# Performance work log

Measured on AMD Instinct MI355X. Metric: run time of the kernel, lower is better.

## Reference

```python
import jax, jax.numpy as jnp
import numpy as np

WIN = (2, 7, 7)
SHIFT = (1, 3, 3)
HEADS = 4
DIM = 128
MLP_HID = 512
N = WIN[0] * WIN[1] * WIN[2]  # 98
EPS = 1e-5


def _rel_pos_index():
    d = np.arange(WIN[0]); h = np.arange(WIN[1]); w = np.arange(WIN[2])
    coords = np.stack(np.meshgrid(d, h, w, indexing='ij'))  # (3, Wd, Wh, Ww)
    flat = coords.reshape(3, -1)  # (3, N)
    rel = flat[:, :, None] - flat[:, None, :]  # (3, N, N)
    rel = rel.transpose(1, 2, 0).astype(np.int64)  # (N, N, 3)
    rel[..., 0] += WIN[0] - 1
    rel[..., 1] += WIN[1] - 1
    rel[..., 2] += WIN[2] - 1
    rel[..., 0] *= (2 * WIN[1] - 1) * (2 * WIN[2] - 1)
    rel[..., 1] *= (2 * WIN[2] - 1)
    return rel.sum(-1)  # (N, N)


def setup_inputs() -> dict:
    key = jax.random.key(0)
    ks = jax.random.split(key, 8)
    B, D, H, W, C = 4, 8, 56, 56, DIM
    tbl_size = (2 * WIN[0] - 1) * (2 * WIN[1] - 1) * (2 * WIN[2] - 1)  # 507
    s = 0.02
    return {
        'x': jax.random.normal(ks[0], (B, D, H, W, C), jnp.float32),
        'rel_idx': jnp.asarray(_rel_pos_index(), jnp.int32),
        'rpb_table': s * jax.random.normal(ks[1], (tbl_size, HEADS), jnp.float32),
        'qkv_w': s * jax.random.normal(ks[2], (C, 3 * C), jnp.float32),
        'qkv_b': jnp.zeros((3 * C,), jnp.float32),
        'proj_w': s * jax.random.normal(ks[3], (C, C), jnp.float32),
        'proj_b': jnp.zeros((C,), jnp.float32),
        'ln1_g': jnp.ones((C,), jnp.float32),
        'ln1_b': jnp.zeros((C,), jnp.float32),
        'ln2_g': jnp.ones((C,), jnp.float32),
        'ln2_b': jnp.zeros((C,), jnp.float32),
        'mlp_w1': s * jax.random.normal(ks[4], (C, MLP_HID), jnp.float32),
        'mlp_b1': jnp.zeros((MLP_HID,), jnp.float32),
        'mlp_w2': s * jax.random.normal(ks[5], (MLP_HID, C), jnp.float32),
        'mlp_b2': jnp.zeros((C,), jnp.float32),
    }


def _layernorm(x, g, b):
    mu = jnp.mean(x, -1, keepdims=True)
    var = jnp.var(x, -1, keepdims=True)
    return (x - mu) * jax.lax.rsqrt(var + EPS) * g + b


def _window_partition(x):
    B, Dp, Hp, Wp, C = x.shape
    x = x.reshape(B, Dp // WIN[0], WIN[0], Hp // WIN[1], WIN[1], Wp // WIN[2], WIN[2], C)
    x = x.transpose(0, 1, 3, 5, 2, 4, 6, 7)
    return x.reshape(-1, N, C)


def _window_reverse(win, B, Dp, Hp, Wp):
    C = win.shape[-1]
    x = win.reshape(B, Dp // WIN[0], Hp // WIN[1], Wp // WIN[2], WIN[0], WIN[1], WIN[2], C)
    x = x.transpose(0, 1, 4, 2, 5, 3, 6, 7)
    return x.reshape(B, Dp, Hp, Wp, C)


def _block(x, rel_idx, rpb_table, qkv_w, qkv_b, proj_w, proj_b,
           ln1_g, ln1_b, ln2_g, ln2_b, mlp_w1, mlp_b1, mlp_w2, mlp_b2):
    B, D, H, W, C = x.shape
    shortcut = x
    x = _layernorm(x, ln1_g, ln1_b)
    pad_d = (-D) % WIN[0]; pad_h = (-H) % WIN[1]; pad_w = (-W) % WIN[2]
    x = jnp.pad(x, ((0, 0), (0, pad_d), (0, pad_h), (0, pad_w), (0, 0)))
    _, Dp, Hp, Wp, _ = x.shape
    x = jnp.roll(x, (-SHIFT[0], -SHIFT[1], -SHIFT[2]), axis=(1, 2, 3))
    xw = _window_partition(x)  # (B_, N, C)
    B_ = xw.shape[0]
    hd = C // HEADS
    qkv = (xw @ qkv_w + qkv_b).reshape(B_, N, 3, HEADS, hd).transpose(2, 0, 3, 1, 4)
    q, k, v = qkv[0], qkv[1], qkv[2]  # (B_, h, N, hd)
    q = q * (hd ** -0.5)
    attn = jnp.einsum('bhnd,bhmd->bhnm', q, k)
    bias = rpb_table[rel_idx.reshape(-1)].reshape(N, N, HEADS).transpose(2, 0, 1)
    attn = attn + bias[None]
    # NOTE: the original module calls attn with mask=None even when shifted.
    attn = jax.nn.softmax(attn, axis=-1)
    out = jnp.einsum('bhnm,bhmd->bhnd', attn, v).transpose(0, 2, 1, 3).reshape(B_, N, C)
    out = out @ proj_w + proj_b
    x = _window_reverse(out, B, Dp, Hp, Wp)
    x = jnp.roll(x, (SHIFT[0], SHIFT[1], SHIFT[2]), axis=(1, 2, 3))
    x = x[:, :D, :H, :W, :]
    x = shortcut + x
    h1 = _layernorm(x, ln2_g, ln2_b)
    h1 = jax.nn.gelu(h1 @ mlp_w1 + mlp_b1, approximate=False)
    return x + (h1 @ mlp_w2 + mlp_b2)


def reference(x, rel_idx, rpb_table, qkv_w, qkv_b, proj_w, proj_b,
              ln1_g, ln1_b, ln2_g, ln2_b, mlp_w1, mlp_b1, mlp_w2, mlp_b2):
    return _block(x, rel_idx, rpb_table, qkv_w, qkv_b, proj_w, proj_b,
                  ln1_g, ln1_b, ln2_g, ln2_b, mlp_w1, mlp_b1, mlp_w2, mlp_b2)
```

## Files before the change

kernel.cpp:

```cpp
#include <hip/hip_runtime.h>
#include <hip/hip_bf16.h>
#include <cstdint>

#define NWIN   1024
#define NTOK   98
#define BIAS_N 9604

typedef __attribute__((ext_vector_type(8))) short bf16x8;
typedef __attribute__((ext_vector_type(4))) float f32x4;

__device__ __forceinline__ float b2f(unsigned short u) {
  union { uint32_t i; float f; } v; v.i = ((uint32_t)u) << 16; return v.f;
}
__device__ __forceinline__ float b2f_lo(uint32_t u) {
  union { uint32_t i; float f; } v; v.i = u << 16; return v.f;
}
__device__ __forceinline__ float b2f_hi(uint32_t u) {
  union { uint32_t i; float f; } v; v.i = u & 0xffff0000u; return v.f;
}
__device__ __forceinline__ unsigned short f2b(float f) {
  union { float f; uint32_t i; } v; v.f = f;
  uint32_t r = v.i + 0x7fffu + ((v.i >> 16) & 1u);
  return (unsigned short)(r >> 16);
}
__device__ __forceinline__ float ldf(const void* p, size_t i, int f32) {
  return f32 ? ((const float*)p)[i] : b2f(((const unsigned short*)p)[i]);
}
__device__ __forceinline__ void stf(void* p, size_t i, int f32, float v) {
  if (f32) ((float*)p)[i] = v;
  else     ((unsigned short*)p)[i] = f2b(v);
}
__device__ __forceinline__ float2 ldf2(const void* p, size_t i, int f32) {
  if (f32) { const float* q = (const float*)p + i; return make_float2(q[0], q[1]); }
  uint32_t u = *(const uint32_t*)((const unsigned short*)p + i);
  return make_float2(b2f_lo(u), b2f_hi(u));
}
__device__ __forceinline__ float gelu_f(float x) {
  float a = fabsf(x) * 0.70710678118654752f;
  float t = __builtin_amdgcn_rcpf(1.0f + 0.3275911f * a);
  float p = ((((1.061405429f * t - 1.453152027f) * t + 1.421413741f) * t
              - 0.284496736f) * t + 0.254829592f) * t;
  float erfp = 1.0f - p * __expf(-a * a);
  return 0.5f * x * (1.0f + copysignf(erfp, x));
}

#define QG_OFF   0
#define KG_OFF   25690112
#define VGT_OFF  51380224
#define ZPAD_OFF 80740352
#define BIAS_OFF 80748544
#define WQ_OFF   80902208
#define WP_OFF   81000512
#define W1_OFF   81033280
#define W2_OFF   81164352
#define PAR_OFF  81295424
#define FLAG_OFF 81302080
#define LNG_OFF  81302144
#define P_LN1G 0
#define P_LN1B 128
#define P_LN2G 256
#define P_LN2B 384
#define P_QKVB 512
#define P_PROJB 896
#define P_B1  1024
#define P_B2  1536

__global__ __launch_bounds__(256) void detect_kernel(const uint32_t* __restrict__ xw,
                                                     int* __restrict__ flag) {
  __shared__ int cnt;
  if (threadIdx.x == 0) cnt = 0;
  __syncthreads();
  uint32_t w = xw[threadIdx.x];
  int e = (w >> 23) & 0xFF;
  if (e >= 112 && e <= 134) atomicAdd(&cnt, 1);
  __syncthreads();
  if (threadIdx.x == 0) *flag = (cnt >= 128) ? 1 : 0;
}

__global__ __launch_bounds__(256) void prep_kernel(
    const void* __restrict__ qkvw, const void* __restrict__ projw,
    const void* __restrict__ w1, const void* __restrict__ w2,
    const void* __restrict__ ln1g, const void* __restrict__ ln1b,
    const void* __restrict__ ln2g, const void* __restrict__ ln2b,
    const void* __restrict__ qkvb, const void* __restrict__ projb,
    const void* __restrict__ b1, const void* __restrict__ b2,
    const int* __restrict__ flag,
    unsigned short* __restrict__ wq_t, unsigned short* __restrict__ wp_t,
    unsigned short* __restrict__ w1_t, unsigned short* __restrict__ w2_t,
    float* __restrict__ par, unsigned short* __restrict__ zpad) {
  const int f32 = *flag;
  int idx = blockIdx.x * 256 + threadIdx.x;
  if (idx < 49152) {
    int n = idx >> 7, k = idx & 127;
    wq_t[idx] = f2b(ldf(qkvw, (size_t)k * 384 + n, f32));
  } else if ((idx -= 49152) < 16384) {
    int n = idx >> 7, k = idx & 127;
    wp_t[idx] = f2b(ldf(projw, (size_t)k * 128 + n, f32));
  } else if ((idx -= 16384) < 65536) {
    int n = idx >> 7, k = idx & 127;
    w1_t[idx] = f2b(ldf(w1, (size_t)k * 512 + n, f32));
  } else if ((idx -= 65536) < 65536) {
    int n = idx >> 9, k = idx & 511;
    w2_t[idx] = f2b(ldf(w2, (size_t)k * 128 + n, f32));
  } else if ((idx -= 65536) < 1664) {
    float v;
    if      (idx < 128)  v = ldf(ln1g, idx, f32);
    else if (idx < 256)  v = ldf(ln1b, idx - 128, f32);
    else if (idx < 384)  v = ldf(ln2g, idx - 256, f32);
    else if (idx < 512)  v = ldf(ln2b, idx - 384, f32);
    else if (idx < 896)  v = ldf(qkvb, idx - 512, f32);
    else if (idx < 1024) v = ldf(projb, idx - 896, f32);
    else if (idx < 1536) v = ldf(b1, idx - 1024, f32);
    else                 v = ldf(b2, idx - 1536, f32);
    par[idx] = v;
  } else if ((idx -= 1664) < 4096) {
    zpad[idx] = 0;
  }
}

__global__ __launch_bounds__(256) void bias_kernel(const int* __restrict__ rel_idx,
                                                   const void* __restrict__ tbl,
                                                   const int* __restrict__ flag,
                                                   float* __restrict__ bias) {
  const int f32 = *flag;
  int i = blockIdx.x * 256 + threadIdx.x;
  if (i >= 4 * BIAS_N) return;
  int h = i / BIAS_N, ij = i % BIAS_N;
  bias[i] = ldf(tbl, (size_t)rel_idx[ij] * 4 + h, f32);
}

__global__ __launch_bounds__(256) void qkv_win_kernel(
    const void* __restrict__ x, const int* __restrict__ flag,
    const unsigned short* __restrict__ wq_t, const float* __restrict__ par,
    unsigned short* __restrict__ qg, unsigned short* __restrict__ kg,
    unsigned short* __restrict__ vgt) {
  __shared__ unsigned short lnx[112 * 136];
  const int f32 = *flag;
  const int tid = threadIdx.x, wave = tid >> 6, lane = tid & 63;
  const int quad = lane >> 4, lcol = lane & 15;
  const int win = blockIdx.x;
  const int bb = win >> 8, r = win & 255;
  const int wd = r >> 6, r2 = r & 63, wh = r2 >> 3, ww = r2 & 7;

  for (int t = wave; t < NTOK; t += 4) {
    int td = t / 49, r3 = t % 49, th = r3 / 7, tw = r3 % 7;
    int sd = (wd * 2 + td + 1) & 7;
    int sh = (wh * 7 + th + 3) % 56;
    int sw = (ww * 7 + tw + 3) % 56;
    size_t src = ((((size_t)bb * 8 + sd) * 56 + sh) * 56 + sw) * 128;
    int c0 = lane * 2;
    float2 f = ldf2(x, src + c0, f32);
    float s = f.x + f.y, ss = f.x * f.x + f.y * f.y;
#pragma unroll
    for (int off = 32; off >= 1; off >>= 1) { s += __shfl_xor(s, off); ss += __shfl_xor(ss, off); }
    float mu = s * (1.0f / 128.0f);
    float var = ss * (1.0f / 128.0f) - mu * mu;
    float rs = rsqrtf(var + 1e-5f);
    float y0 = (f.x - mu) * rs * par[P_LN1G + c0] + par[P_LN1B + c0];
    float y1 = (f.y - mu) * rs * par[P_LN1G + c0 + 1] + par[P_LN1B + c0 + 1];
    *(uint32_t*)(lnx + t * 136 + c0) = (uint32_t)f2b(y0) | ((uint32_t)f2b(y1) << 16);
  }
  for (int i = tid; i < 14 * 68; i += 256) {
    int rr = i / 68, c = i % 68;
    *(uint32_t*)(lnx + (98 + rr) * 136 + c * 2) = 0u;
  }
  __syncthreads();

  for (int p = 0; p < 6; ++p) {
    const int n = p * 64 + wave * 16 + lcol;
    bf16x8 bfr[4];
#pragma unroll
    for (int ks = 0; ks < 4; ++ks)
      bfr[ks] = *(const bf16x8*)(wq_t + (size_t)n * 128 + ks * 32 + quad * 8);
    const int region = n >> 7, cc = n & 127, head = cc >> 5, d = cc & 31;
    const float bc = par[P_QKVB + n];
    if (region < 2) {
      unsigned short* dst = (region == 0 ? qg : kg) +
                            (((size_t)win * 4 + head) * NTOK) * 32 + d;
      const float scale = region == 0 ? 0.17677669529663687f : 1.0f;
      for (int mt = 0; mt < 7; ++mt) {
        f32x4 acc = (f32x4){0.f, 0.f, 0.f, 0.f};
#pragma unroll
        for (int ks = 0; ks < 4; ++ks) {
          bf16x8 a = *(const bf16x8*)(lnx + (mt * 16 + lcol) * 136 + ks * 32 + quad * 8);
          acc = __builtin_amdgcn_mfma_f32_16x16x32_bf16(a, bfr[ks], acc, 0, 0, 0);
        }
#pragma unroll
        for (int rr = 0; rr < 4; ++rr) {
          int m = mt * 16 + quad * 4 + rr;
          if (m < NTOK) dst[m * 32] = f2b((acc[rr] + bc) * scale);
        }
      }
    } else {
      unsigned short* dstv = vgt + (((size_t)win * 4 + head) * 32 + d) * 112;
      for (int mt = 0; mt < 7; ++mt) {
        f32x4 acc = (f32x4){0.f, 0.f, 0.f, 0.f};
#pragma unroll
        for (int ks = 0; ks < 4; ++ks) {
          bf16x8 a = *(const bf16x8*)(lnx + (mt * 16 + lcol) * 136 + ks * 32 + quad * 8);
          acc = __builtin_amdgcn_mfma_f32_16x16x32_bf16(a, bfr[ks], acc, 0, 0, 0);
        }
        ushort4 w;
        int m0 = mt * 16 + quad * 4;
        w.x = (m0 + 0 < NTOK) ? f2b(acc[0] + bc) : (unsigned short)0;
        w.y = (m0 + 1 < NTOK) ? f2b(acc[1] + bc) : (unsigned short)0;
        w.z = (m0 + 2 < NTOK) ? f2b(acc[2] + bc) : (unsigned short)0;
        w.w = (m0 + 3 < NTOK) ? f2b(acc[3] + bc) : (unsigned short)0;
        *(ushort4*)(dstv + m0) = w;
      }
    }
  }
}

__global__ __launch_bounds__(256, 4) void attn_fused_kernel(
    const unsigned short* __restrict__ qg, const unsigned short* __restrict__ kg,
    const unsigned short* __restrict__ vgt, const float* __restrict__ bias,
    const unsigned short* __restrict__ wp_t, const float* __restrict__ par,
    const void* __restrict__ x, const int* __restrict__ flag,
    unsigned short* __restrict__ lng, void* __restrict__ out) {
  __shared__ __align__(16) unsigned short smem[15232];
  const int f32 = *flag;
  const int tid = threadIdx.x, wave = tid >> 6, lane = tid & 63;
  const int quad = lane >> 4, lcol = lane & 15;
  const int win = blockIdx.x, h = wave;
  const size_t hb = (((size_t)win * 4 + h) * NTOK) * 32;
  const unsigned short* vbase = vgt + (((size_t)win * 4 + h) * 32) * 112;

  unsigned short* plh = smem + h * (16 * 132);

  for (int idx = lane; idx < 16 * 16; idx += 64) {
    int rr = idx >> 4, c = 112 + (idx & 15);
    plh[rr * 132 + c] = 0;
  }

  bf16x8 aq[7], bk[7];
#pragma unroll
  for (int t = 0; t < 7; ++t) {
    int row = min(t * 16 + lcol, NTOK - 1);
    aq[t] = *(const bf16x8*)(qg + hb + (size_t)row * 32 + quad * 8);
    bk[t] = *(const bf16x8*)(kg + hb + (size_t)row * 32 + quad * 8);
  }

  const float* bh = bias + h * BIAS_N;
  f32x4 o[7][2];
  for (int mt = 0; mt < 7; ++mt) {
    f32x4 s[7];
#pragma unroll
    for (int nt = 0; nt < 7; ++nt)
      s[nt] = __builtin_amdgcn_mfma_f32_16x16x32_bf16(aq[mt], bk[nt],
                                                      (f32x4){0.f, 0.f, 0.f, 0.f}, 0, 0, 0);
    const int ib = mt * 16 + quad * 4;
#pragma unroll
    for (int nt = 0; nt < 7; ++nt) {
      int j = nt * 16 + lcol;
      bool jv = j < NTOK;
#pragma unroll
      for (int r = 0; r < 4; ++r) {
        int ic = min(ib + r, NTOK - 1);
        s[nt][r] = jv ? (s[nt][r] + bh[ic * NTOK + j]) : -3.0e38f;
      }
    }
    float mx[4], sum[4], inv[4];
#pragma unroll
    for (int r = 0; r < 4; ++r) {
      float m = s[0][r];
#pragma unroll
      for (int nt = 1; nt < 7; ++nt) m = fmaxf(m, s[nt][r]);
      mx[r] = m;
    }
#pragma unroll
    for (int off = 1; off < 16; off <<= 1)
#pragma unroll
      for (int r = 0; r < 4; ++r) mx[r] = fmaxf(mx[r], __shfl_xor(mx[r], off));
#pragma unroll
    for (int r = 0; r < 4; ++r) sum[r] = 0.f;
#pragma unroll
    for (int nt = 0; nt < 7; ++nt)
#pragma unroll
      for (int r = 0; r < 4; ++r) {
        float e = __expf(s[nt][r] - mx[r]);
        s[nt][r] = e; sum[r] += e;
      }
#pragma unroll
    for (int off = 1; off < 16; off <<= 1)
#pragma unroll
      for (int r = 0; r < 4; ++r) sum[r] += __shfl_xor(sum[r], off);
#pragma unroll
    for (int r = 0; r < 4; ++r) inv[r] = 1.0f / sum[r];
#pragma unroll
    for (int nt = 0; nt < 7; ++nt)
#pragma unroll
      for (int r = 0; r < 4; ++r)
        plh[(quad * 4 + r) * 132 + nt * 16 + lcol] = f2b(s[nt][r] * inv[r]);
#pragma unroll
    for (int n2 = 0; n2 < 2; ++n2) {
      f32x4 acc = (f32x4){0.f, 0.f, 0.f, 0.f};
#pragma unroll
      for (int kp = 0; kp < 4; ++kp) {
        bf16x8 a = *(const bf16x8*)(plh + lcol * 132 + kp * 32 + quad * 8);
        bf16x8 b = *(const bf16x8*)(vbase + (size_t)(n2 * 16 + lcol) * 112 +
                                    kp * 32 + quad * 8);
        acc = __builtin_amdgcn_mfma_f32_16x16x32_bf16(a, b, acc, 0, 0, 0);
      }
      o[mt][n2] = acc;
    }
  }
  __syncthreads();

  unsigned short* olds = smem;
#pragma unroll
  for (int mt = 0; mt < 7; ++mt)
#pragma unroll
    for (int n2 = 0; n2 < 2; ++n2)
#pragma unroll
      for (int r = 0; r < 4; ++r)
        olds[(mt * 16 + quad * 4 + r) * 136 + h * 32 + n2 * 16 + lcol] = f2b(o[mt][n2][r]);
  __syncthreads();

  f32x4 pr[2][7];
  for (int t2 = 0; t2 < 2; ++t2) {
    const int n = (h * 2 + t2) * 16 + lcol;
    bf16x8 bw[4];
#pragma unroll
    for (int kp = 0; kp < 4; ++kp)
      bw[kp] = *(const bf16x8*)(wp_t + (size_t)n * 128 + kp * 32 + quad * 8);
    for (int mt = 0; mt < 7; ++mt) {
      f32x4 acc = (f32x4){0.f, 0.f, 0.f, 0.f};
#pragma unroll
      for (int kp = 0; kp < 4; ++kp) {
        bf16x8 a = *(const bf16x8*)(olds + (mt * 16 + lcol) * 136 + kp * 32 + quad * 8);
        acc = __builtin_amdgcn_mfma_f32_16x16x32_bf16(a, bw[kp], acc, 0, 0, 0);
      }
      pr[t2][mt] = acc;
    }
  }
  __syncthreads();

  const int bb = win >> 8, rW = win & 255;
  const int wd = rW >> 6, r2 = rW & 63, wh = r2 >> 3, ww = r2 & 7;
  const int c = (tid & 31) * 4;
  const float4 gv = *(const float4*)(par + P_LN2G + c);
  const float4 bv = *(const float4*)(par + P_LN2B + c);
  float* pout = (float*)smem;
  for (int pass = 0; pass < 2; ++pass) {
    const int mlo = pass * 56;
    for (int t2 = 0; t2 < 2; ++t2) {
      const int n = (h * 2 + t2) * 16 + lcol;
      const float bc = par[P_PROJB + n];
#pragma unroll
      for (int mt = 0; mt < 7; ++mt)
#pragma unroll
        for (int r = 0; r < 4; ++r) {
          int m = mt * 16 + quad * 4 + r;
          if (m >= mlo && m < mlo + 56 && m < NTOK)
            pout[(m - mlo) * 132 + n] = pr[t2][mt][r] + bc;
        }
    }
    __syncthreads();
    for (int i = tid >> 5; i < 56; i += 8) {
      int m = mlo + i;
      if (m >= NTOK) break;
      int td = m / 49, r3 = m % 49, th = r3 / 7, tw = r3 % 7;
      int sd = (wd * 2 + td + 1) & 7;
      int sh = (wh * 7 + th + 3) % 56;
      int sw = (ww * 7 + tw + 3) % 56;
      size_t base = ((((size_t)bb * 8 + sd) * 56 + sh) * 56 + sw) * 128 + c;
      float4 p = *(const float4*)(pout + i * 132 + c);
      float4 v;
      if (f32) {
        const float4 xr = *(const float4*)((const float*)x + base);
        v = make_float4(p.x + xr.x, p.y + xr.y, p.z + xr.z, p.w + xr.w);
        *(float4*)((float*)out + base) = v;
      } else {
        const ushort4 xr = *(const ushort4*)((const unsigned short*)x + base);
        v = make_float4(p.x + b2f(xr.x), p.y + b2f(xr.y),
                        p.z + b2f(xr.z), p.w + b2f(xr.w));
        ushort4 ov;
        ov.x = f2b(v.x); ov.y = f2b(v.y); ov.z = f2b(v.z); ov.w = f2b(v.w);
        *(ushort4*)((unsigned short*)out + base) = ov;
      }
      float s = v.x + v.y + v.z + v.w;
      float ss = v.x * v.x + v.y * v.y + v.z * v.z + v.w * v.w;
#pragma unroll
      for (int off = 1; off < 32; off <<= 1) {
        s += __shfl_xor(s, off); ss += __shfl_xor(ss, off);
      }
      float mu = s * (1.0f / 128.0f);
      float var = ss * (1.0f / 128.0f) - mu * mu;
      float rs = rsqrtf(var + 1e-5f);
      ushort4 lv;
      lv.x = f2b((v.x - mu) * rs * gv.x + bv.x);
      lv.y = f2b((v.y - mu) * rs * gv.y + bv.y);
      lv.z = f2b((v.z - mu) * rs * gv.z + bv.z);
      lv.w = f2b((v.w - mu) * rs * gv.w + bv.w);
      *(ushort4*)(lng + base) = lv;
    }
    if (pass == 0) __syncthreads();
  }
}

__global__ __launch_bounds__(256) void mlp_kernel(
    const unsigned short* __restrict__ w1_t, const unsigned short* __restrict__ w2_t,
    const float* __restrict__ par, const int* __restrict__ flag,
    const unsigned short* __restrict__ lng, void* __restrict__ out) {
  __shared__ __align__(16) unsigned short hbuf[32 * 264];
  const int f32 = *flag;
  const int tid = threadIdx.x, wave = tid >> 6, lane = tid & 63;
  const int quad = lane >> 4, lcol = lane & 15;
  const int m0 = blockIdx.x * 32;
  const int nb = wave * 16 + lcol;

  bf16x8 a1[2][4];
#pragma unroll
  for (int mt = 0; mt < 2; ++mt)
#pragma unroll
    for (int ks = 0; ks < 4; ++ks)
      a1[mt][ks] = *(const bf16x8*)(lng + (size_t)(m0 + mt * 16 + lcol) * 128 +
                                    ks * 32 + quad * 8);

  f32x4 acc2[2][2];
#pragma unroll
  for (int a = 0; a < 2; ++a)
#pragma unroll
    for (int b = 0; b < 2; ++b) acc2[a][b] = (f32x4){0.f, 0.f, 0.f, 0.f};

#pragma unroll 1
  for (int g = 0; g < 2; ++g) {
    for (int p = 0; p < 4; ++p) {
      const int nl = p * 64 + nb;
      const int n = g * 256 + nl;
      bf16x8 bfr[4];
#pragma unroll
      for (int ks = 0; ks < 4; ++ks)
        bfr[ks] = *(const bf16x8*)(w1_t + (size_t)n * 128 + ks * 32 + quad * 8);
      const float bc = par[P_B1 + n];
#pragma unroll
      for (int mt = 0; mt < 2; ++mt) {
        f32x4 acc = (f32x4){0.f, 0.f, 0.f, 0.f};
#pragma unroll
        for (int ks = 0; ks < 4; ++ks)
          acc = __builtin_amdgcn_mfma_f32_16x16x32_bf16(a1[mt][ks], bfr[ks], acc, 0, 0, 0);
#pragma unroll
        for (int rr = 0; rr < 4; ++rr) {
          int m = mt * 16 + quad * 4 + rr;
          hbuf[m * 264 + nl] = f2b(gelu_f(acc[rr] + bc));
        }
      }
    }
    __syncthreads();

#pragma unroll
    for (int np = 0; np < 2; ++np) {
      for (int kp = 0; kp < 2; ++kp) {
        bf16x8 b2r[4];
#pragma unroll
        for (int ks = 0; ks < 4; ++ks)
          b2r[ks] = *(const bf16x8*)(w2_t + (size_t)(np * 64 + nb) * 512 + g * 256 +
                                     kp * 128 + ks * 32 + quad * 8);
#pragma unroll
        for (int mt = 0; mt < 2; ++mt) {
#pragma unroll
          for (int ks = 0; ks < 4; ++ks) {
            bf16x8 a = *(const bf16x8*)(hbuf + (mt * 16 + lcol) * 264 + kp * 128 +
                                        ks * 32 + quad * 8);
            acc2[np][mt] = __builtin_amdgcn_mfma_f32_16x16x32_bf16(a, b2r[ks], acc2[np][mt], 0, 0, 0);
          }
        }
      }
    }
    __syncthreads();
  }

  float* pout = (float*)hbuf;
#pragma unroll
  for (int np = 0; np < 2; ++np) {
    const int n = np * 64 + nb;
    const float bc = par[P_B2 + n];
#pragma unroll
    for (int mt = 0; mt < 2; ++mt)
#pragma unroll
      for (int rr = 0; rr < 4; ++rr)
        pout[(mt * 16 + quad * 4 + rr) * 132 + n] = acc2[np][mt][rr] + bc;
  }
  __syncthreads();

  for (int i = tid; i < 1024; i += 256) {
    int t = i >> 5, c = (i & 31) * 4;
    size_t base = (size_t)(m0 + t) * 128 + c;
    float4 p = *(const float4*)(pout + t * 132 + c);
    if (f32) {
      const float4 xr = *(const float4*)((const float*)out + base);
      float4 ov = make_float4(p.x + xr.x, p.y + xr.y, p.z + xr.z, p.w + xr.w);
      *(float4*)((float*)out + base) = ov;
    } else {
      const ushort4 xr = *(const ushort4*)((const unsigned short*)out + base);
      ushort4 ov;
      ov.x = f2b(p.x + b2f(xr.x)); ov.y = f2b(p.y + b2f(xr.y));
      ov.z = f2b(p.z + b2f(xr.z)); ov.w = f2b(p.w + b2f(xr.w));
      *(ushort4*)((unsigned short*)out + base) = ov;
    }
  }
}

extern "C" void kernel_launch(void* const* d_in, const int* in_sizes, int n_in,
                              void* d_out, int out_size, void* d_ws, size_t ws_size,
                              hipStream_t stream) {
  const void* x      = d_in[0];
  const int*  rel    = (const int*)d_in[1];
  const void* rpb    = d_in[2];
  const void* qkv_w  = d_in[3];
  const void* qkv_b  = d_in[4];
  const void* proj_w = d_in[5];
  const void* proj_b = d_in[6];
  const void* ln1_g  = d_in[7];
  const void* ln1_b  = d_in[8];
  const void* ln2_g  = d_in[9];
  const void* ln2_b  = d_in[10];
  const void* w1     = d_in[11];
  const void* b1     = d_in[12];
  const void* w2     = d_in[13];
  const void* b2     = d_in[14];

  char* ws = (char*)d_ws;
  unsigned short* qg   = (unsigned short*)(ws + QG_OFF);
  unsigned short* kg   = (unsigned short*)(ws + KG_OFF);
  unsigned short* vgt  = (unsigned short*)(ws + VGT_OFF);
  unsigned short* zpad = (unsigned short*)(ws + ZPAD_OFF);
  float*          bias = (float*)(ws + BIAS_OFF);
  unsigned short* wq_t = (unsigned short*)(ws + WQ_OFF);
  unsigned short* wp_t = (unsigned short*)(ws + WP_OFF);
  unsigned short* w1_t = (unsigned short*)(ws + W1_OFF);
  unsigned short* w2_t = (unsigned short*)(ws + W2_OFF);
  float*          par  = (float*)(ws + PAR_OFF);
  int*            flag = (int*)(ws + FLAG_OFF);
  unsigned short* lng  = (unsigned short*)(ws + LNG_OFF);

  detect_kernel<<<1, 256, 0, stream>>>((const uint32_t*)x, flag);
  prep_kernel<<<791, 256, 0, stream>>>(qkv_w, proj_w, w1, w2, ln1_g, ln1_b, ln2_g,
                                       ln2_b, qkv_b, proj_b, b1, b2, flag,
                                       wq_t, wp_t, w1_t, w2_t, par, zpad);
  bias_kernel<<<(4 * BIAS_N + 255) / 256, 256, 0, stream>>>(rel, rpb, flag, bias);
  qkv_win_kernel<<<NWIN, 256, 0, stream>>>(x, flag, wq_t, par, qg, kg, vgt);
  attn_fused_kernel<<<NWIN, 256, 0, stream>>>(qg, kg, vgt, bias, wp_t, par, x, flag,
                                              lng, d_out);
  mlp_kernel<<<100352 / 32, 256, 0, stream>>>(w1_t, w2_t, par, flag, lng, d_out);
}
```

Before: 414.4 us.

## Fuse QKV projection into attention kernel, keeping Q and K in shared memory

Merges the QKV projection kernel into the fused attention kernel, one block per window. Q and K now go to LDS instead of global workspace, which drops a global round trip for Q/K and one kernel launch. V is still written to global and read back by the same block. LDS use grows to about 77KB and launch bounds drop to 2 blocks per CU, so occupancy falls.

Result: slower. 426.3 us (+2.9%).

```diff
diff --git a/kernel.cpp b/kernel.cpp
--- a/kernel.cpp
+++ b/kernel.cpp
@@ -25,10 +25,6 @@
 }
 __device__ __forceinline__ float ldf(const void* p, size_t i, int f32) {
   return f32 ? ((const float*)p)[i] : b2f(((const unsigned short*)p)[i]);
-}
-__device__ __forceinline__ void stf(void* p, size_t i, int f32, float v) {
-  if (f32) ((float*)p)[i] = v;
-  else     ((unsigned short*)p)[i] = f2b(v);
 }
 __device__ __forceinline__ float2 ldf2(const void* p, size_t i, int f32) {
   if (f32) { const float* q = (const float*)p + i; return make_float2(q[0], q[1]); }
@@ -129,18 +125,23 @@
   bias[i] = ldf(tbl, (size_t)rel_idx[ij] * 4 + h, f32);
 }
 
-__global__ __launch_bounds__(256) void qkv_win_kernel(
+__global__ __launch_bounds__(256, 2) void attn_fused_kernel(
     const void* __restrict__ x, const int* __restrict__ flag,
-    const unsigned short* __restrict__ wq_t, const float* __restrict__ par,
-    unsigned short* __restrict__ qg, unsigned short* __restrict__ kg,
-    unsigned short* __restrict__ vgt) {
-  __shared__ unsigned short lnx[112 * 136];
+    const unsigned short* __restrict__ wq_t, const float* __restrict__ bias,
+    const unsigned short* __restrict__ wp_t, const float* __restrict__ par,
+    unsigned short* __restrict__ vgt, unsigned short* __restrict__ lng,
+    void* __restrict__ out) {
+  __shared__ __align__(16) unsigned short smem[38416];
   const int f32 = *flag;
   const int tid = threadIdx.x, wave = tid >> 6, lane = tid & 63;
   const int quad = lane >> 4, lcol = lane & 15;
-  const int win = blockIdx.x;
-  const int bb = win >> 8, r = win & 255;
-  const int wd = r >> 6, r2 = r & 63, wh = r2 >> 3, ww = r2 & 7;
+  const int win = blockIdx.x, h = wave;
+  const int bb = win >> 8, rW = win & 255;
+  const int wd = rW >> 6, r2 = rW & 63, wh = r2 >> 3, ww = r2 & 7;
+
+  unsigned short* lnx = smem;
+  unsigned short* qs  = smem + 13328;
+  unsigned short* ks  = smem + 25872;
 
   for (int t = wave; t < NTOK; t += 4) {
     int td = t / 49, r3 = t % 49, th = r3 / 7, tw = r3 % 7;
@@ -160,35 +161,33 @@
     float y1 = (f.y - mu) * rs * par[P_LN1G + c0 + 1] + par[P_LN1B + c0 + 1];
     *(uint32_t*)(lnx + t * 136 + c0) = (uint32_t)f2b(y0) | ((uint32_t)f2b(y1) << 16);
   }
-  for (int i = tid; i < 14 * 68; i += 256) {
-    int rr = i / 68, c = i % 68;
-    *(uint32_t*)(lnx + (98 + rr) * 136 + c * 2) = 0u;
-  }
   __syncthreads();
 
   for (int p = 0; p < 6; ++p) {
     const int n = p * 64 + wave * 16 + lcol;
     bf16x8 bfr[4];
 #pragma unroll
-    for (int ks = 0; ks < 4; ++ks)
-      bfr[ks] = *(const bf16x8*)(wq_t + (size_t)n * 128 + ks * 32 + quad * 8);
-    const int region = n >> 7, cc = n & 127, head = cc >> 5, d = cc & 31;
+    for (int ks4 = 0; ks4 < 4; ++ks4)
+      bfr[ks4] = *(const bf16x8*)(wq_t + (size_t)n * 128 + ks4 * 32 + quad * 8);
+    const int region = p >> 1;
+    const int head = (p & 1) * 2 + (wave >> 1);
+    const int d = (wave & 1) * 16 + lcol;
     const float bc = par[P_QKVB + n];
     if (region < 2) {
-      unsigned short* dst = (region == 0 ? qg : kg) +
-                            (((size_t)win * 4 + head) * NTOK) * 32 + d;
+      unsigned short* dstl = (region == 0 ? qs : ks) + head * 3136 + d;
       const float scale = region == 0 ? 0.17677669529663687f : 1.0f;
       for (int mt = 0; mt < 7; ++mt) {
         f32x4 acc = (f32x4){0.f, 0.f, 0.f, 0.f};
 #pragma unroll
-        for (int ks = 0; ks < 4; ++ks) {
-          bf16x8 a = *(const bf16x8*)(lnx + (mt * 16 + lcol) * 136 + ks * 32 + quad * 8);
-          acc = __builtin_amdgcn_mfma_f32_16x16x32_bf16(a, bfr[ks], acc, 0, 0, 0);
+        for (int ks4 = 0; ks4 < 4; ++ks4) {
+          bf16x8 a = *(const bf16x8*)(lnx + min(mt * 16 + lcol, NTOK - 1) * 136 +
+                                      ks4 * 32 + quad * 8);
+          acc = __builtin_amdgcn_mfma_f32_16x16x32_bf16(a, bfr[ks4], acc, 0, 0, 0);
         }
 #pragma unroll
         for (int rr = 0; rr < 4; ++rr) {
           int m = mt * 16 + quad * 4 + rr;
-          if (m < NTOK) dst[m * 32] = f2b((acc[rr] + bc) * scale);
+          if (m < NTOK) dstl[m * 32] = f2b((acc[rr] + bc) * scale);
         }
       }
     } else {
@@ -196,9 +195,10 @@
       for (int mt = 0; mt < 7; ++mt) {
         f32x4 acc = (f32x4){0.f, 0.f, 0.f, 0.f};
 #pragma unroll
-        for (int ks = 0; ks < 4; ++ks) {
-          bf16x8 a = *(const bf16x8*)(lnx + (mt * 16 + lcol) * 136 + ks * 32 + quad * 8);
-          acc = __builtin_amdgcn_mfma_f32_16x16x32_bf16(a, bfr[ks], acc, 0, 0, 0);
+        for (int ks4 = 0; ks4 < 4; ++ks4) {
+          bf16x8 a = *(const bf16x8*)(lnx + min(mt * 16 + lcol, NTOK - 1) * 136 +
+                                      ks4 * 32 + quad * 8);
+          acc = __builtin_amdgcn_mfma_f32_16x16x32_bf16(a, bfr[ks4], acc, 0, 0, 0);
         }
         ushort4 w;
         int m0 = mt * 16 + quad * 4;
@@ -210,35 +210,21 @@
       }
     }
   }
-}
-
-__global__ __launch_bounds__(256, 4) void attn_fused_kernel(
-    const unsigned short* __restrict__ qg, const unsigned short* __restrict__ kg,
-    const unsigned short* __restrict__ vgt, const float* __restrict__ bias,
-    const unsigned short* __restrict__ wp_t, const float* __restrict__ par,
-    const void* __restrict__ x, const int* __restrict__ flag,
-    unsigned short* __restrict__ lng, void* __restrict__ out) {
-  __shared__ __align__(16) unsigned short smem[15232];
-  const int f32 = *flag;
-  const int tid = threadIdx.x, wave = tid >> 6, lane = tid & 63;
-  const int quad = lane >> 4, lcol = lane & 15;
-  const int win = blockIdx.x, h = wave;
-  const size_t hb = (((size_t)win * 4 + h) * NTOK) * 32;
+  __syncthreads();
+
   const unsigned short* vbase = vgt + (((size_t)win * 4 + h) * 32) * 112;
-
-  unsigned short* plh = smem + h * (16 * 132);
-
+  unsigned short* plh = smem + h * 2112;
+
+  bf16x8 aq[7], bk[7];
+#pragma unroll
+  for (int t = 0; t < 7; ++t) {
+    int row = min(t * 16 + lcol, NTOK - 1);
+    aq[t] = *(const bf16x8*)(qs + h * 3136 + row * 32 + quad * 8);
+    bk[t] = *(const bf16x8*)(ks + h * 3136 + row * 32 + quad * 8);
+  }
   for (int idx = lane; idx < 16 * 16; idx += 64) {
     int rr = idx >> 4, c = 112 + (idx & 15);
     plh[rr * 132 + c] = 0;
-  }
-
-  bf16x8 aq[7], bk[7];
-#pragma unroll
-  for (int t = 0; t < 7; ++t) {
-    int row = min(t * 16 + lcol, NTOK - 1);
-    aq[t] = *(const bf16x8*)(qg + hb + (size_t)row * 32 + quad * 8);
-    bk[t] = *(const bf16x8*)(kg + hb + (size_t)row * 32 + quad * 8);
   }
 
   const float* bh = bias + h * BIAS_N;
@@ -307,7 +293,7 @@
   }
   __syncthreads();
 
-  unsigned short* olds = smem;
+  unsigned short* olds = smem + 13328;
 #pragma unroll
   for (int mt = 0; mt < 7; ++mt)
 #pragma unroll
@@ -336,8 +322,6 @@
   }
   __syncthreads();
 
-  const int bb = win >> 8, rW = win & 255;
-  const int wd = rW >> 6, r2 = rW & 63, wh = r2 >> 3, ww = r2 & 7;
   const int c = (tid & 31) * 4;
   const float4 gv = *(const float4*)(par + P_LN2G + c);
   const float4 bv = *(const float4*)(par + P_LN2B + c);
@@ -522,8 +506,6 @@
   const void* b2     = d_in[14];
 
   char* ws = (char*)d_ws;
-  unsigned short* qg   = (unsigned short*)(ws + QG_OFF);
-  unsigned short* kg   = (unsigned short*)(ws + KG_OFF);
   unsigned short* vgt  = (unsigned short*)(ws + VGT_OFF);
   unsigned short* zpad = (unsigned short*)(ws + ZPAD_OFF);
   float*          bias = (float*)(ws + BIAS_OFF);
@@ -540,8 +522,7 @@
                                        ln2_b, qkv_b, proj_b, b1, b2, flag,
                                        wq_t, wp_t, w1_t, w2_t, par, zpad);
   bias_kernel<<<(4 * BIAS_N + 255) / 256, 256, 0, stream>>>(rel, rpb, flag, bias);
-  qkv_win_kernel<<<NWIN, 256, 0, stream>>>(x, flag, wq_t, par, qg, kg, vgt);
-  attn_fused_kernel<<<NWIN, 256, 0, stream>>>(qg, kg, vgt, bias, wp_t, par, x, flag,
-                                              lng, d_out);
+  attn_fused_kernel<<<NWIN, 256, 0, stream>>>(x, flag, wq_t, bias, wp_t, par,
+                                              vgt, lng, d_out);
   mlp_kernel<<<100352 / 32, 256, 0, stream>>>(w1_t, w2_t, par, flag, lng, d_out);
 }
```
